# Optimization experiments

Hardware: AMD Instinct MI355X
Metric: run time of the kernel (lower is better)

Reference implementation:

```python
import jax, jax.numpy as jnp
import numpy as np

INF = 1e8
STRIDES = (8, 16, 32, 64, 128)
SIZES_OF_INTEREST = ((0.0, 80.0), (64.0, 160.0), (128.0, 320.0), (256.0, 640.0), (512.0, 1e7))
LEVEL_HW = ((128, 128), (64, 64), (32, 32), (16, 16), (8, 8))
B, N_BOX = 4, 64
MIN_RADIUS2 = 16.0          # min_radius ** 2
DELTA = (1 - 0.8) / (1 + 0.8)
ALPHA, BETA, GAMMA = 0.25, 4.0, 2.0
SIGMOID_CLAMP = 1e-4
IGNORE_HIGH_FP = 0.85
POS_W = NEG_W = 0.5
REG_WEIGHT = 1.0


def _static():
    grids, strides, ranges, loc = [], [], [], []
    for (h, w), s, (lo, hi) in zip(LEVEL_HW, STRIDES, SIZES_OF_INTEREST):
        ys, xs = np.meshgrid(np.arange(h) * s, np.arange(w) * s, indexing='ij')
        g = np.stack([xs.reshape(-1), ys.reshape(-1)], 1).astype(np.float32) + s // 2
        grids.append(g)
        strides.append(np.full(h * w, s, np.float32))
        ranges.append(np.broadcast_to(np.array([lo, hi], np.float32), (h * w, 2)).copy())
        loc.append(h * w)
    loc = np.array(loc)
    bases = np.concatenate([[0], np.cumsum(loc * B)])[:-1]
    return np.concatenate(grids), np.concatenate(strides), np.concatenate(ranges), loc, bases

_G, _S, _R, LOC_PER_LEVEL, LEVEL_BASES = _static()
GRIDS = jnp.asarray(_G)          # [M_img, 2]
STRIDE_VEC = jnp.asarray(_S)     # [M_img]
SIZE_RANGES = jnp.asarray(_R)    # [M_img, 2]
M_IMG = GRIDS.shape[0]
M_TOT = B * M_IMG


def _assign_one(boxes):
    """GT assignment for one image. boxes [N,4] -> (reg_targets [M,4], agn_hm [M])."""
    l = GRIDS[:, 0:1] - boxes[None, :, 0]
    t = GRIDS[:, 1:2] - boxes[None, :, 1]
    r = boxes[None, :, 2] - GRIDS[:, 0:1]
    b = boxes[None, :, 3] - GRIDS[:, 1:2]
    reg = jnp.stack([l, t, r, b], 2)                              # [M,N,4]
    centers = (boxes[:, :2] + boxes[:, 2:]) / 2                   # [N,2]
    s = STRIDE_VEC[:, None, None]                                 # [M,1,1]
    cdis = (centers[None] / s).astype(jnp.int32).astype(jnp.float32) * s + s / 2  # [M,N,2]
    diff = GRIDS[:, None, :] - cdis                               # [M,N,2]
    is_peak = (diff ** 2).sum(-1) == 0
    is_in = reg.min(2) > 0
    c3x3 = (jnp.abs(diff[..., 0]) <= s[..., 0]) & (jnp.abs(diff[..., 1]) <= s[..., 0]) & is_in
    crit = jnp.sqrt(((reg[:, :, :2] + reg[:, :, 2:]) ** 2).sum(2)) / 2
    cared = (crit >= SIZE_RANGES[:, 0:1]) & (crit <= SIZE_RANGES[:, 1:2])
    reg_mask = c3x3 & cared
    dist2 = ((GRIDS[:, None, :] - centers[None]) ** 2).sum(-1)
    dist2 = jnp.where(is_peak, 0.0, dist2)
    area = (boxes[:, 2] - boxes[:, 0]) * (boxes[:, 3] - boxes[:, 1])
    radius2 = jnp.maximum(DELTA ** 2 * 2 * area, MIN_RADIUS2)
    wdist2 = dist2 / radius2[None]                                # [M,N]
    d = jnp.where(reg_mask, wdist2, INF)
    min_d = d.min(1)
    min_i = d.argmin(1)
    rt = jnp.take_along_axis(reg, min_i[:, None, None], 1)[:, 0, :]
    rt = jnp.where((min_d >= INF)[:, None], -INF, rt)
    hm = jnp.exp(-wdist2.min(1))
    hm = jnp.where(hm < 1e-4, 0.0, hm)
    return rt / STRIDE_VEC[:, None], hm


def _to_level_major(x):
    """[B, M_img, ...] -> [B*M_img, ...] in level-major (level, image, loc) order == _transpose."""
    outs, start = [], 0
    for m in LOC_PER_LEVEL:
        outs.append(x[:, start:start + int(m)].reshape((B * int(m),) + x.shape[2:]))
        start += int(m)
    return jnp.concatenate(outs, 0)


def _pos_inds(boxes):
    """_get_label_inds: flat positive indices [B*N*L] plus validity mask."""
    centers = (boxes[..., :2] + boxes[..., 2:]) / 2               # [B,N,2]
    st = jnp.asarray(STRIDES, jnp.float32)
    ci = (centers[:, :, None, :] / st[None, None, :, None]).astype(jnp.int32)  # [B,N,L,2]
    Ws = jnp.asarray([w for (_, w) in LEVEL_HW])
    loc = jnp.asarray(LOC_PER_LEVEL)
    bases = jnp.asarray(LEVEL_BASES)
    im = jnp.arange(B)[:, None, None]
    pos = bases[None, None, :] + im * loc[None, None, :] + ci[..., 1] * Ws[None, None, :] + ci[..., 0]
    crit = jnp.sqrt(((boxes[..., 2:] - boxes[..., :2]) ** 2).sum(-1)) / 2     # [B,N]
    lo = jnp.asarray([r[0] for r in SIZES_OF_INTEREST])
    hi = jnp.asarray([r[1] for r in SIZES_OF_INTEREST])
    mask = (crit[..., None] >= lo) & (crit[..., None] <= hi)
    return pos.reshape(-1), mask.reshape(-1)


def _giou_loss(pred, target):
    pl, pt, pr, pb = pred[:, 0], pred[:, 1], pred[:, 2], pred[:, 3]
    tl, tt, tr, tb = target[:, 0], target[:, 1], target[:, 2], target[:, 3]
    target_area = (tl + tr) * (tt + tb)
    pred_area = (pl + pr) * (pt + pb)
    w_i = jnp.minimum(pl, tl) + jnp.minimum(pr, tr)
    g_w = jnp.maximum(pl, tl) + jnp.maximum(pr, tr)
    h_i = jnp.minimum(pb, tb) + jnp.minimum(pt, tt)
    g_h = jnp.maximum(pb, tb) + jnp.maximum(pt, tt)
    ac = g_w * g_h + 1e-7
    inter = w_i * h_i
    union = target_area + pred_area - inter
    ious = (inter + 1.0) / (union + 1.0)
    gious = ious - (ac - union) / ac
    return 1.0 - gious


def _losses(boxes, agn_hm_pred, reg_pred):
    reg_targets, hms = jax.vmap(_assign_one)(boxes)               # [B,M,4], [B,M]
    reg_targets = _to_level_major(reg_targets)                    # [M_tot,4]
    hm = _to_level_major(hms)                                     # [M_tot]
    pos_inds, pos_mask = _pos_inds(boxes)
    num_pos_avg = jnp.maximum(pos_mask.sum().astype(jnp.float32), 1.0)

    reg_valid = reg_targets.max(1) >= 0
    safe_t = jnp.where(reg_valid[:, None], reg_targets, 1.0)
    reg_norm = jnp.maximum(reg_valid.sum().astype(jnp.float32), 1.0)
    reg_loss = REG_WEIGHT * jnp.sum(jnp.where(reg_valid, _giou_loss(reg_pred, safe_t), 0.0)) / reg_norm

    # binary heatmap focal loss (class-agnostic)
    pred = jnp.clip(jax.nn.sigmoid(agn_hm_pred), SIGMOID_CLAMP, 1.0 - SIGMOID_CLAMP)
    neg_w = jnp.power(1.0 - hm, BETA)
    idx = jnp.clip(pos_inds, 0, M_TOT - 1)
    pos_pred = pred[idx]
    pos_terms = jnp.where(pos_mask, jnp.log(pos_pred) * jnp.power(1.0 - pos_pred, GAMMA), 0.0)
    neg_terms = jnp.log(1.0 - pred) * jnp.power(pred, GAMMA) * neg_w
    neg_terms = jnp.where(pred < IGNORE_HIGH_FP, neg_terms, 0.0)
    agn_pos = POS_W * (ALPHA * (-pos_terms.sum())) / num_pos_avg
    agn_neg = NEG_W * ((1.0 - ALPHA) * (-neg_terms.sum())) / num_pos_avg
    return jnp.stack([reg_loss, agn_pos, agn_neg])


def setup_inputs() -> dict:
    key = jax.random.key(0)
    k1, k2, k3, k4, k5 = jax.random.split(key, 5)
    cxy = jax.random.uniform(k1, (B, N_BOX, 2), minval=40.0, maxval=984.0)
    wh = jax.random.uniform(k2, (B, N_BOX, 2), minval=16.0, maxval=512.0)
    boxes = jnp.concatenate([jnp.clip(cxy - wh / 2, 0.0, 1024.0),
                             jnp.clip(cxy + wh / 2, 0.0, 1024.0)], -1)
    gt_classes = jax.random.randint(k3, (B, N_BOX), 0, 4)
    agn_hm_pred = jax.random.normal(k4, (M_TOT,), jnp.float32) * 2.0 - 3.0
    reg_pred = jax.random.uniform(k5, (M_TOT, 4), jnp.float32) * 6.0 + 0.1
    return {"boxes": boxes, "gt_classes": gt_classes,
            "agn_hm_pred": agn_hm_pred, "reg_pred": reg_pred}


def reference(boxes, gt_classes, agn_hm_pred, reg_pred):
    # gt_classes unused: only_proposal=True -> class-agnostic heatmap path
    return _losses(boxes, agn_hm_pred, reg_pred)
```

## Files before the change

kernel.cpp:

```cpp
#include <hip/hip_runtime.h>
#include <math.h>

#define M_TOT 87296
#define NMAIN 682
#define INF_F 100000000.0f


__global__ __launch_bounds__(256, 3) void main_kernel(
    const float* __restrict__ boxes,
    const float* __restrict__ agn,
    const float* __restrict__ reg_pred,
    float* __restrict__ ws)
{
    __shared__ float4 sBox[256];
    __shared__ float  sRed[16];

    const int t   = threadIdx.x;
    const int blk = blockIdx.x;

    const int   LB_[5]   = {0, 65536, 81920, 86016, 87040};
    const int   locSh[5] = {14, 12, 10, 8, 6};
    const int   wSh[5]   = {7, 6, 5, 4, 3};
    const float SV[5]    = {8.f, 16.f, 32.f, 64.f, 128.f};
    const float LOv[5]   = {0.f, 64.f, 128.f, 256.f, 512.f};
    const float HIv[5]   = {80.f, 160.f, 320.f, 640.f, 10000000.f};

    if (blk == NMAIN) {
        const int   LOC[5] = {16384, 4096, 1024, 256, 64};
        const int   WW[5]  = {128, 64, 32, 16, 8};
        float psum = 0.f, pcnt = 0.f;
        for (int j = t; j < 1280; j += 256) {
            const int lev = j % 5;
            const int bn  = j / 5;
            const int b   = bn >> 6;
            const float4 bx = ((const float4*)boxes)[bn];
            const float cx = (bx.x + bx.z) * 0.5f;
            const float cy = (bx.y + bx.w) * 0.5f;
            const int cix = (int)(cx / SV[lev]);
            const int ciy = (int)(cy / SV[lev]);
            int pos = LB_[lev] + b * LOC[lev] + ciy * WW[lev] + cix;
            pos = min(max(pos, 0), M_TOT - 1);
            const float dx = bx.z - bx.x, dy = bx.w - bx.y;
            const float crit = sqrtf(dx * dx + dy * dy) * 0.5f;
            const bool msk = (crit >= LOv[lev]) && (crit <= HIv[lev]);
            const float z = agn[pos];
            float pp = 1.0f / (1.0f + expf(-z));
            pp = fminf(fmaxf(pp, 1e-4f), 1.0f - 1e-4f);
            if (msk) {
                const float om = 1.0f - pp;
                psum += logf(pp) * (om * om);
                pcnt += 1.0f;
            }
        }
        for (int off = 32; off; off >>= 1) {
            psum += __shfl_down(psum, off);
            pcnt += __shfl_down(pcnt, off);
        }
        if ((t & 63) == 0) { sRed[t >> 6] = psum; sRed[4 + (t >> 6)] = pcnt; }
        __syncthreads();
        if (t == 0) {
            ws[3 * NMAIN]     = sRed[0] + sRed[1] + sRed[2] + sRed[3];
            ws[3 * NMAIN + 1] = sRed[4] + sRed[5] + sRed[6] + sRed[7];
        }
        return;
    }

    const int mbase = blk << 7;
    int lev;
    if      (mbase < 65536) lev = 0;
    else if (mbase < 81920) lev = 1;
    else if (mbase < 86016) lev = 2;
    else if (mbase < 87040) lev = 3;
    else                    lev = 4;

    const int   LB    = LB_[lev];
    const int   lsh   = locSh[lev];
    const int   wsh   = wSh[lev];
    const float s     = SV[lev];
    const float inv_s = 1.0f / s;
    const float half  = 0.5f * s;
    const float lo    = LOv[lev], hi = HIv[lev];

    sBox[t] = ((const float4*)boxes)[t];
    __syncthreads();

    const int g       = t >> 3;
    const int su      = t & 7;
    const int locBase = mbase + g * 4;
    const int imgBase = ((locBase - LB) >> lsh) << 6;
    const int p0      = (locBase - LB) & ((1 << lsh) - 1);
    const float gx0   = (float)(p0 & ((1 << wsh) - 1)) * s + half;
    const float gy    = (float)(p0 >> wsh) * s + half;

    float  zEarly  = 0.f;
    float4 pvEarly = make_float4(0.f, 0.f, 0.f, 0.f);
    if (su < 4) {
        zEarly  = agn[locBase + su];
        pvEarly = ((const float4*)reg_pred)[locBase + su];
    }

    const double DELTA = (1.0 - 0.8) / (1.0 + 0.8);
    const float  RADC  = (float)(DELTA * DELTA * 2.0);

    float l0[8], rr0[8], ttbb[8], dx0[8], ddx0[8], ddy2[8], bir[8];
    bool  yok[8], ypk[8];
    #pragma unroll
    for (int k = 0; k < 8; ++k) {
        const float4 A = sBox[imgBase + su + 8 * k];
        const float bcx = (A.x + A.z) * 0.5f;
        const float bcy = (A.y + A.w) * 0.5f;
        const float bqx = truncf(bcx * inv_s) * s + half;
        const float bqy = truncf(bcy * inv_s) * s + half;
        l0[k]  = gx0 - A.x;
        rr0[k] = A.z - gx0;
        const float tt = gy - A.y;
        const float bb = A.w - gy;
        ttbb[k] = fminf(tt, bb);
        dx0[k]  = gx0 - bqx;
        const float dyc = gy - bqy;
        ddx0[k] = gx0 - bcx;
        const float ddy = gy - bcy;
        ddy2[k] = ddy * ddy;
        const float bw = A.z - A.x, bh = A.w - A.y;
        const float area = bw * bh;
        bir[k] = 1.0f / fmaxf(RADC * area, 16.0f);
        const float crit = sqrtf(bw * bw + bh * bh) * 0.5f;
        yok[k] = (fabsf(dyc) <= s) && (crit >= lo) && (crit <= hi);
        ypk[k] = (dyc == 0.0f);
    }

    float minW[4], bestD[4];
    int   bestN[4];
    #pragma unroll
    for (int j = 0; j < 4; ++j) { minW[j] = INF_F; bestD[j] = INF_F; bestN[j] = 0; }

    #pragma unroll
    for (int k = 0; k < 8; ++k) {
        const float tb  = ttbb[k];
        const float b_  = bir[k];
        const float dy2 = ddy2[k];
        const bool  yk  = yok[k];
        const bool  pk  = ypk[k];
        const int   n   = su + 8 * k;
        #pragma unroll
        for (int j = 0; j < 4; ++j) {
            const float js  = (float)j * s;
            const float l   = l0[k] + js;
            const float rr  = rr0[k] - js;
            const float dx  = dx0[k] + js;
            const float ddx = ddx0[k] + js;
            const bool is_in = fminf(fminf(l, rr), tb) > 0.0f;
            const bool xok   = fabsf(dx) <= s;
            const bool peak  = (dx == 0.0f) && pk;
            const bool msk   = is_in && xok && yk;
            float dist2 = ddx * ddx + dy2;
            dist2 = peak ? 0.0f : dist2;
            const float w2 = dist2 * b_;
            minW[j] = fminf(minW[j], w2);
            const float d = msk ? w2 : INF_F;
            if (d < bestD[j]) { bestD[j] = d; bestN[j] = n; }
        }
    }

    unsigned long long myKey = ~0ULL; float myMinW = INF_F;
    #pragma unroll
    for (int j = 0; j < 4; ++j) {
        unsigned long long kj =
            ((unsigned long long)__float_as_uint(bestD[j]) << 6) | (unsigned)bestN[j];
        float wj = minW[j];
        #pragma unroll
        for (int m = 1; m < 8; m <<= 1) {
            const unsigned long long o = __shfl_xor(kj, m);
            kj = o < kj ? o : kj;
            wj = fminf(wj, __shfl_xor(wj, m));
        }
        if (su == j) { myKey = kj; myMinW = wj; }
    }

    float neg_term = 0.f, reg_term = 0.f, reg_val = 0.f;
    if (su < 4) {
        float hmv = expf(-myMinW);
        if (hmv < 1e-4f) hmv = 0.0f;
        const float u = 1.0f - hmv;
        const float neg_w = (u * u) * (u * u);
        float pr = 1.0f / (1.0f + expf(-zEarly));
        pr = fminf(fmaxf(pr, 1e-4f), 1.0f - 1e-4f);
        if (pr < 0.85f) neg_term = logf(1.0f - pr) * (pr * pr) * neg_w;

        if ((unsigned)(myKey >> 6) < __float_as_uint(INF_F)) {
            reg_val = 1.0f;
            const int n = (int)(myKey & 63);
            const float4 A = sBox[imgBase + n];
            const int   px = (p0 & ((1 << wsh) - 1)) + su;
            const float gx = (float)px * s + half;
            const float tl  = (gx - A.x) * inv_s;
            const float tt2 = (gy - A.y) * inv_s;
            const float tr  = (A.z - gx) * inv_s;
            const float tb2 = (A.w - gy) * inv_s;
            const float pl = pvEarly.x, pt = pvEarly.y, prr = pvEarly.z, pb = pvEarly.w;
            const float target_area = (tl + tr) * (tt2 + tb2);
            const float pred_area   = (pl + prr) * (pt + pb);
            const float w_i = fminf(pl, tl) + fminf(prr, tr);
            const float g_w = fmaxf(pl, tl) + fmaxf(prr, tr);
            const float h_i = fminf(pb, tb2) + fminf(pt, tt2);
            const float g_h = fmaxf(pb, tb2) + fmaxf(pt, tt2);
            const float ac    = g_w * g_h + 1e-7f;
            const float inter = w_i * h_i;
            const float uni   = target_area + pred_area - inter;
            const float ious  = (inter + 1.0f) / (uni + 1.0f);
            const float gious = ious - (ac - uni) / ac;
            reg_term = 1.0f - gious;
        }
    }

    float r0 = reg_term, r1 = reg_val, r2 = neg_term;
    for (int off = 32; off; off >>= 1) {
        r0 += __shfl_down(r0, off);
        r1 += __shfl_down(r1, off);
        r2 += __shfl_down(r2, off);
    }
    if ((t & 63) == 0) {
        const int w = t >> 6;
        sRed[w * 3 + 0] = r0; sRed[w * 3 + 1] = r1; sRed[w * 3 + 2] = r2;
    }
    __syncthreads();
    if (t == 0) {
        ws[blk]             = sRed[0] + sRed[3] + sRed[6] + sRed[9];
        ws[NMAIN + blk]     = sRed[1] + sRed[4] + sRed[7] + sRed[10];
        ws[2 * NMAIN + blk] = sRed[2] + sRed[5] + sRed[8] + sRed[11];
    }
}

__global__ __launch_bounds__(256) void finalize(
    const float* __restrict__ ws,
    float* __restrict__ out)
{
    const int t = threadIdx.x;
    float racc = 0.f, cacc = 0.f, nacc = 0.f;
    for (int j = t; j < NMAIN; j += 256) {
        racc += ws[j];
        cacc += ws[NMAIN + j];
        nacc += ws[2 * NMAIN + j];
    }
    for (int off = 32; off; off >>= 1) {
        racc += __shfl_down(racc, off);
        cacc += __shfl_down(cacc, off);
        nacc += __shfl_down(nacc, off);
    }
    __shared__ float sr[4][3];
    if ((t & 63) == 0) {
        const int w = t >> 6;
        sr[w][0] = racc; sr[w][1] = cacc; sr[w][2] = nacc;
    }
    __syncthreads();
    if (t == 0) {
        const float RS = sr[0][0] + sr[1][0] + sr[2][0] + sr[3][0];
        const float RC = sr[0][1] + sr[1][1] + sr[2][1] + sr[3][1];
        const float NS = sr[0][2] + sr[1][2] + sr[2][2] + sr[3][2];
        const float PS = ws[3 * NMAIN];
        const float PC = ws[3 * NMAIN + 1];
        const float num_pos  = fmaxf(PC, 1.0f);
        const float reg_norm = fmaxf(RC, 1.0f);
        out[0] = RS / reg_norm;
        out[1] = 0.5f * (0.25f * -PS) / num_pos;
        out[2] = 0.5f * (0.75f * -NS) / num_pos;
    }
}

extern "C" void kernel_launch(void* const* d_in, const int* in_sizes, int n_in,
                              void* d_out, int out_size, void* d_ws, size_t ws_size,
                              hipStream_t stream) {
    const float* boxes    = (const float*)d_in[0];
    const float* agn      = (const float*)d_in[2];
    const float* reg_pred = (const float*)d_in[3];
    float* out = (float*)d_out;
    float* ws  = (float*)d_ws;

    main_kernel<<<NMAIN + 1, 256, 0, stream>>>(boxes, agn, reg_pred, ws);
    finalize<<<1, 256, 0, stream>>>(ws, out);
}
```

Before: 70.02 us.

## Fuse main and finalize kernels via cooperative launch with grid sync

Merges the per-block reduction kernel and the single-block finalize kernel into one cooperative kernel that uses a grid-wide barrier before block 0 performs the final reduction. Workspace writes and reads become agent-scope atomic operations so the values are visible across the barrier. The goal is to remove the second kernel launch and its launch gap. In exchange, the whole kernel pays for a grid sync, and the cooperative launch requires all 683 blocks to be co-resident. If that launch fails, the code falls back to the original two-kernel path.

```diff
diff --git a/kernel.cpp b/kernel.cpp
--- a/kernel.cpp
+++ b/kernel.cpp
@@ -1,69 +1,79 @@
 #include <hip/hip_runtime.h>
+#include <hip/hip_cooperative_groups.h>
 #include <math.h>
+
+namespace cg = cooperative_groups;
 
 #define M_TOT 87296
 #define NMAIN 682
 #define INF_F 100000000.0f
-
-
-__global__ __launch_bounds__(256, 3) void main_kernel(
-    const float* __restrict__ boxes,
-    const float* __restrict__ agn,
-    const float* __restrict__ reg_pred,
-    float* __restrict__ ws)
-{
-    __shared__ float4 sBox[256];
-    __shared__ float  sRed[16];
-
-    const int t   = threadIdx.x;
-    const int blk = blockIdx.x;
-
+#define SCOPE_AGENT __HIP_MEMORY_SCOPE_AGENT
+
+
+__device__ __forceinline__ void pos_work(const float* __restrict__ boxes,
+                                         const float* __restrict__ agn,
+                                         float* __restrict__ ws,
+                                         const int t, float* sRed)
+{
+    const int   LB_[5]   = {0, 65536, 81920, 86016, 87040};
+    const float SV[5]    = {8.f, 16.f, 32.f, 64.f, 128.f};
+    const float LOv[5]   = {0.f, 64.f, 128.f, 256.f, 512.f};
+    const float HIv[5]   = {80.f, 160.f, 320.f, 640.f, 10000000.f};
+    const int   LOC[5]   = {16384, 4096, 1024, 256, 64};
+    const int   WW[5]    = {128, 64, 32, 16, 8};
+    float psum = 0.f, pcnt = 0.f;
+    for (int j = t; j < 1280; j += 256) {
+        const int lev = j % 5;
+        const int bn  = j / 5;
+        const int b   = bn >> 6;
+        const float4 bx = ((const float4*)boxes)[bn];
+        const float cx = (bx.x + bx.z) * 0.5f;
+        const float cy = (bx.y + bx.w) * 0.5f;
+        const int cix = (int)(cx / SV[lev]);
+        const int ciy = (int)(cy / SV[lev]);
+        int pos = LB_[lev] + b * LOC[lev] + ciy * WW[lev] + cix;
+        pos = min(max(pos, 0), M_TOT - 1);
+        const float dx = bx.z - bx.x, dy = bx.w - bx.y;
+        const float crit = sqrtf(dx * dx + dy * dy) * 0.5f;
+        const bool msk = (crit >= LOv[lev]) && (crit <= HIv[lev]);
+        const float z = agn[pos];
+        float pp = 1.0f / (1.0f + expf(-z));
+        pp = fminf(fmaxf(pp, 1e-4f), 1.0f - 1e-4f);
+        if (msk) {
+            const float om = 1.0f - pp;
+            psum += logf(pp) * (om * om);
+            pcnt += 1.0f;
+        }
+    }
+    for (int off = 32; off; off >>= 1) {
+        psum += __shfl_down(psum, off);
+        pcnt += __shfl_down(pcnt, off);
+    }
+    if ((t & 63) == 0) { sRed[t >> 6] = psum; sRed[4 + (t >> 6)] = pcnt; }
+    __syncthreads();
+    if (t == 0) {
+        __hip_atomic_store(&ws[3 * NMAIN],
+                           sRed[0] + sRed[1] + sRed[2] + sRed[3],
+                           __ATOMIC_RELAXED, SCOPE_AGENT);
+        __hip_atomic_store(&ws[3 * NMAIN + 1],
+                           sRed[4] + sRed[5] + sRed[6] + sRed[7],
+                           __ATOMIC_RELAXED, SCOPE_AGENT);
+    }
+}
+
+__device__ __forceinline__ void main_work(const float* __restrict__ boxes,
+                                          const float* __restrict__ agn,
+                                          const float* __restrict__ reg_pred,
+                                          float* __restrict__ ws,
+                                          const int t, const int blk,
+                                          float4* sBox, float* sRed)
+{
     const int   LB_[5]   = {0, 65536, 81920, 86016, 87040};
     const int   locSh[5] = {14, 12, 10, 8, 6};
     const int   wSh[5]   = {7, 6, 5, 4, 3};
     const float SV[5]    = {8.f, 16.f, 32.f, 64.f, 128.f};
     const float LOv[5]   = {0.f, 64.f, 128.f, 256.f, 512.f};
     const float HIv[5]   = {80.f, 160.f, 320.f, 640.f, 10000000.f};
-
-    if (blk == NMAIN) {
-        const int   LOC[5] = {16384, 4096, 1024, 256, 64};
-        const int   WW[5]  = {128, 64, 32, 16, 8};
-        float psum = 0.f, pcnt = 0.f;
-        for (int j = t; j < 1280; j += 256) {
-            const int lev = j % 5;
-            const int bn  = j / 5;
-            const int b   = bn >> 6;
-            const float4 bx = ((const float4*)boxes)[bn];
-            const float cx = (bx.x + bx.z) * 0.5f;
-            const float cy = (bx.y + bx.w) * 0.5f;
-            const int cix = (int)(cx / SV[lev]);
-            const int ciy = (int)(cy / SV[lev]);
-            int pos = LB_[lev] + b * LOC[lev] + ciy * WW[lev] + cix;
-            pos = min(max(pos, 0), M_TOT - 1);
-            const float dx = bx.z - bx.x, dy = bx.w - bx.y;
-            const float crit = sqrtf(dx * dx + dy * dy) * 0.5f;
-            const bool msk = (crit >= LOv[lev]) && (crit <= HIv[lev]);
-            const float z = agn[pos];
-            float pp = 1.0f / (1.0f + expf(-z));
-            pp = fminf(fmaxf(pp, 1e-4f), 1.0f - 1e-4f);
-            if (msk) {
-                const float om = 1.0f - pp;
-                psum += logf(pp) * (om * om);
-                pcnt += 1.0f;
-            }
-        }
-        for (int off = 32; off; off >>= 1) {
-            psum += __shfl_down(psum, off);
-            pcnt += __shfl_down(pcnt, off);
-        }
-        if ((t & 63) == 0) { sRed[t >> 6] = psum; sRed[4 + (t >> 6)] = pcnt; }
-        __syncthreads();
-        if (t == 0) {
-            ws[3 * NMAIN]     = sRed[0] + sRed[1] + sRed[2] + sRed[3];
-            ws[3 * NMAIN + 1] = sRed[4] + sRed[5] + sRed[6] + sRed[7];
-        }
-        return;
-    }
 
     const int mbase = blk << 7;
     int lev;
@@ -225,46 +235,92 @@
     }
     __syncthreads();
     if (t == 0) {
-        ws[blk]             = sRed[0] + sRed[3] + sRed[6] + sRed[9];
-        ws[NMAIN + blk]     = sRed[1] + sRed[4] + sRed[7] + sRed[10];
-        ws[2 * NMAIN + blk] = sRed[2] + sRed[5] + sRed[8] + sRed[11];
-    }
-}
-
-__global__ __launch_bounds__(256) void finalize(
-    const float* __restrict__ ws,
-    float* __restrict__ out)
-{
-    const int t = threadIdx.x;
+        __hip_atomic_store(&ws[blk],             sRed[0] + sRed[3] + sRed[6] + sRed[9],
+                           __ATOMIC_RELAXED, SCOPE_AGENT);
+        __hip_atomic_store(&ws[NMAIN + blk],     sRed[1] + sRed[4] + sRed[7] + sRed[10],
+                           __ATOMIC_RELAXED, SCOPE_AGENT);
+        __hip_atomic_store(&ws[2 * NMAIN + blk], sRed[2] + sRed[5] + sRed[8] + sRed[11],
+                           __ATOMIC_RELAXED, SCOPE_AGENT);
+    }
+}
+
+__device__ __forceinline__ void final_work(const float* __restrict__ ws,
+                                           float* __restrict__ out,
+                                           const int t, float* sr)
+{
     float racc = 0.f, cacc = 0.f, nacc = 0.f;
     for (int j = t; j < NMAIN; j += 256) {
-        racc += ws[j];
-        cacc += ws[NMAIN + j];
-        nacc += ws[2 * NMAIN + j];
+        racc += __hip_atomic_load(&ws[j],             __ATOMIC_RELAXED, SCOPE_AGENT);
+        cacc += __hip_atomic_load(&ws[NMAIN + j],     __ATOMIC_RELAXED, SCOPE_AGENT);
+        nacc += __hip_atomic_load(&ws[2 * NMAIN + j], __ATOMIC_RELAXED, SCOPE_AGENT);
     }
     for (int off = 32; off; off >>= 1) {
         racc += __shfl_down(racc, off);
         cacc += __shfl_down(cacc, off);
         nacc += __shfl_down(nacc, off);
     }
-    __shared__ float sr[4][3];
     if ((t & 63) == 0) {
         const int w = t >> 6;
-        sr[w][0] = racc; sr[w][1] = cacc; sr[w][2] = nacc;
+        sr[w * 3 + 0] = racc; sr[w * 3 + 1] = cacc; sr[w * 3 + 2] = nacc;
     }
     __syncthreads();
     if (t == 0) {
-        const float RS = sr[0][0] + sr[1][0] + sr[2][0] + sr[3][0];
-        const float RC = sr[0][1] + sr[1][1] + sr[2][1] + sr[3][1];
-        const float NS = sr[0][2] + sr[1][2] + sr[2][2] + sr[3][2];
-        const float PS = ws[3 * NMAIN];
-        const float PC = ws[3 * NMAIN + 1];
+        const float RS = sr[0] + sr[3] + sr[6] + sr[9];
+        const float RC = sr[1] + sr[4] + sr[7] + sr[10];
+        const float NS = sr[2] + sr[5] + sr[8] + sr[11];
+        const float PS = __hip_atomic_load(&ws[3 * NMAIN],     __ATOMIC_RELAXED, SCOPE_AGENT);
+        const float PC = __hip_atomic_load(&ws[3 * NMAIN + 1], __ATOMIC_RELAXED, SCOPE_AGENT);
         const float num_pos  = fmaxf(PC, 1.0f);
         const float reg_norm = fmaxf(RC, 1.0f);
         out[0] = RS / reg_norm;
         out[1] = 0.5f * (0.25f * -PS) / num_pos;
         out[2] = 0.5f * (0.75f * -NS) / num_pos;
     }
+}
+
+__global__ __launch_bounds__(256, 3) void fused_kernel(
+    const float* __restrict__ boxes,
+    const float* __restrict__ agn,
+    const float* __restrict__ reg_pred,
+    float* __restrict__ ws,
+    float* __restrict__ out)
+{
+    __shared__ float4 sBox[256];
+    __shared__ float  sRed[16];
+    const int t   = threadIdx.x;
+    const int blk = blockIdx.x;
+
+    if (blk == NMAIN) pos_work(boxes, agn, ws, t, sRed);
+    else              main_work(boxes, agn, reg_pred, ws, t, blk, sBox, sRed);
+
+    cg::this_grid().sync();
+
+    if (blk == 0) {
+        __syncthreads();
+        final_work(ws, out, t, sRed);
+    }
+}
+
+__global__ __launch_bounds__(256, 3) void main_kernel(
+    const float* __restrict__ boxes,
+    const float* __restrict__ agn,
+    const float* __restrict__ reg_pred,
+    float* __restrict__ ws)
+{
+    __shared__ float4 sBox[256];
+    __shared__ float  sRed[16];
+    const int t   = threadIdx.x;
+    const int blk = blockIdx.x;
+    if (blk == NMAIN) pos_work(boxes, agn, ws, t, sRed);
+    else              main_work(boxes, agn, reg_pred, ws, t, blk, sBox, sRed);
+}
+
+__global__ __launch_bounds__(256) void finalize(
+    const float* __restrict__ ws,
+    float* __restrict__ out)
+{
+    __shared__ float sr[16];
+    final_work(ws, out, threadIdx.x, sr);
 }
 
 extern "C" void kernel_launch(void* const* d_in, const int* in_sizes, int n_in,
@@ -276,6 +332,12 @@
     float* out = (float*)d_out;
     float* ws  = (float*)d_ws;
 
-    main_kernel<<<NMAIN + 1, 256, 0, stream>>>(boxes, agn, reg_pred, ws);
-    finalize<<<1, 256, 0, stream>>>(ws, out);
-}
+    void* args[] = {(void*)&boxes, (void*)&agn, (void*)&reg_pred, (void*)&ws, (void*)&out};
+    hipError_t e = hipLaunchCooperativeKernel((const void*)fused_kernel,
+                                              dim3(NMAIN + 1), dim3(256),
+                                              args, 0u, stream);
+    if (e != hipSuccess) {
+        main_kernel<<<NMAIN + 1, 256, 0, stream>>>(boxes, agn, reg_pred, ws);
+        finalize<<<1, 256, 0, stream>>>(ws, out);
+    }
+}
```

After: 146.4 us. +109.1%, slower.
